# Optimization experiments

Hardware: AMD Instinct MI355X
Metric: run time of the kernel (lower is better)

The kernel has to match this reference:

```python
import jax, jax.numpy as jnp
import numpy as np

B, T_ENC, T_DEC = 64, 256, 200
MEL, R = 80, 2
ENC_DIM = 256   # must equal attention_context_dim (context = weighted sum of encoder outputs)
ATT = 256       # attention_rnn_units == attention_context_dim
DEC = 256       # decoder_rnn_units
PRE1, PRE2 = 256, 128


def _gru(x, h, wih, whh, bih, bhh):
    # torch.nn.GRUCell math; weights are (3*H, in) torch layout
    gi = x @ wih.T + bih
    gh = h @ whh.T + bhh
    i_r, i_z, i_n = jnp.split(gi, 3, axis=-1)
    h_r, h_z, h_n = jnp.split(gh, 3, axis=-1)
    r = jax.nn.sigmoid(i_r + h_r)
    z = jax.nn.sigmoid(i_z + h_z)
    n = jnp.tanh(i_n + r * h_n)
    return (1.0 - z) * n + z * h


def setup_inputs() -> dict:
    key = jax.random.key(0)
    ks = iter(jax.random.split(key, 40))
    def nrm(shape, s=0.05):
        return jax.random.normal(next(ks), shape, dtype=jnp.float32) * s
    inp = {
        "encoder_outputs": nrm((B, T_ENC, ENC_DIM), 1.0),
        "inputs": nrm((B, T_DEC, MEL * R), 1.0),
        "memory_lengths": jax.random.randint(next(ks), (B,), T_ENC // 2, T_ENC + 1),
        # prenet
        "pre_w1": nrm((PRE1, MEL * R)), "pre_b1": jnp.zeros((PRE1,), jnp.float32),
        "pre_w2": nrm((PRE2, PRE1)),    "pre_b2": jnp.zeros((PRE2,), jnp.float32),
        # memory layer (no bias)
        "mem_w": nrm((ATT, ENC_DIM)),
        # attention GRUCell: input = prenet_out(128) + context(256)
        "att_wih": nrm((3 * ATT, PRE2 + ATT)), "att_whh": nrm((3 * ATT, ATT)),
        "att_bih": jnp.zeros((3 * ATT,), jnp.float32), "att_bhh": jnp.zeros((3 * ATT,), jnp.float32),
        # Bahdanau attention: query layer (no bias) and v vector
        "q_w": nrm((ATT, ATT)), "v_w": nrm((ATT,)),
        # project_to_decoder_in
        "proj_w": nrm((DEC, ATT + ATT)), "proj_b": jnp.zeros((DEC,), jnp.float32),
        # two decoder GRUCells
        "g1_wih": nrm((3 * DEC, DEC)), "g1_whh": nrm((3 * DEC, DEC)),
        "g1_bih": jnp.zeros((3 * DEC,), jnp.float32), "g1_bhh": jnp.zeros((3 * DEC,), jnp.float32),
        "g2_wih": nrm((3 * DEC, DEC)), "g2_whh": nrm((3 * DEC, DEC)),
        "g2_bih": jnp.zeros((3 * DEC,), jnp.float32), "g2_bhh": jnp.zeros((3 * DEC,), jnp.float32),
        # output projections
        "mel_w": nrm((MEL * R, DEC + ATT)), "mel_b": jnp.zeros((MEL * R,), jnp.float32),
        "stop_w": nrm((1, DEC + ATT)),      "stop_b": jnp.zeros((1,), jnp.float32),
    }
    return inp


def reference(encoder_outputs, inputs, memory_lengths,
              pre_w1, pre_b1, pre_w2, pre_b2, mem_w,
              att_wih, att_whh, att_bih, att_bhh, q_w, v_w,
              proj_w, proj_b,
              g1_wih, g1_whh, g1_bih, g1_bhh,
              g2_wih, g2_whh, g2_bih, g2_bhh,
              mel_w, mel_b, stop_w, stop_b):
    b = encoder_outputs.shape[0]
    processed_memory = encoder_outputs @ mem_w.T                    # (B,T_enc,ATT)
    pad_mask = jnp.arange(T_ENC)[None, :] >= memory_lengths[:, None]  # True = padding

    # teacher forcing: step t consumes previous target frame (zeros at t=0)
    x_seq = jnp.concatenate([jnp.zeros((b, 1, MEL * R), inputs.dtype), inputs[:, :-1]], axis=1)
    xs = jnp.swapaxes(x_seq, 0, 1)                                  # (T_dec,B,mel*r)

    def step(carry, x):
        h_att, ctx, h1, h2 = carry
        # prenet (dropout omitted: deterministic reference)
        pre = jax.nn.relu(jax.nn.relu(x @ pre_w1.T + pre_b1) @ pre_w2.T + pre_b2)
        # attention RNN
        h_att = _gru(jnp.concatenate([pre, ctx], -1), h_att, att_wih, att_whh, att_bih, att_bhh)
        # Bahdanau alignment
        score = jnp.einsum('btd,d->bt', jnp.tanh(processed_memory + (h_att @ q_w.T)[:, None, :]), v_w)
        score = jnp.where(pad_mask, -jnp.inf, score)
        align = jax.nn.softmax(score, axis=-1)                      # (B,T_enc)
        ctx = jnp.einsum('bt,btd->bd', align, encoder_outputs)      # (B,ATT)
        # decoder stack with residuals
        d = jnp.concatenate([h_att, ctx], -1) @ proj_w.T + proj_b
        h1 = _gru(d, h1, g1_wih, g1_whh, g1_bih, g1_bhh); d = h1 + d
        h2 = _gru(d, h2, g2_wih, g2_whh, g2_bih, g2_bhh); d = h2 + d
        p = jnp.concatenate([d, ctx], -1)
        mel = p @ mel_w.T + mel_b                                   # (B,mel*r)
        stop = jax.nn.sigmoid(p @ stop_w.T + stop_b)[:, 0]          # (B,)
        return (h_att, ctx, h1, h2), (mel, align, stop)

    zeros = lambda d: jnp.zeros((b, d), encoder_outputs.dtype)
    init = (zeros(ATT), zeros(ATT), zeros(DEC), zeros(DEC))
    _, (mels, aligns, stops) = jax.lax.scan(step, init, xs)

    mel_outputs = jnp.swapaxes(mels, 0, 1)                          # (B,T_dec,mel*r)
    attn_scores = jnp.swapaxes(aligns, 0, 1)                        # (B,T_dec,T_enc)
    stop_tokens = jnp.repeat(jnp.swapaxes(stops, 0, 1), R, axis=1)  # (B,T_dec*r)
    return mel_outputs, attn_scores, stop_tokens
```

## Files before the change

kernel.cpp:

```cpp
#include <hip/hip_runtime.h>
#include <math.h>
#include <stdint.h>

#define NB   64
#define TE   256
#define TD   200
#define MR   160

typedef _Float16 h2 __attribute__((ext_vector_type(2)));

__device__ __forceinline__ float dot2f(h2 a, h2 b, float c){
  return __builtin_amdgcn_fdot2(a, b, c, false);
}
__device__ __forceinline__ h2 u2h(unsigned int u){ return __builtin_bit_cast(h2, u); }
__device__ __forceinline__ unsigned int h2u(h2 h){ return __builtin_bit_cast(unsigned int, h); }
__device__ __forceinline__ unsigned f2u(float f){ return __builtin_bit_cast(unsigned, f); }
__device__ __forceinline__ float u2f(unsigned u){ return __builtin_bit_cast(float, u); }

__device__ __forceinline__ float sigmf(float x){
  return __fdividef(1.f, 1.f + __expf(-x));
}
__device__ __forceinline__ float tanhf_(float x){
  float ax = fabsf(x);
  float e  = __expf(-2.f*ax);
  float r  = __fdividef(1.f - e, 1.f + e);
  return copysignf(r, x);
}

static constexpr size_t OFF_PM   = 0;
static constexpr size_t OFF_ENCH = 8388608;
static constexpr size_t OFF_GIP  = 16777216;
static constexpr size_t OFF_P    = 36438016;
static constexpr size_t OFF_W2   = 49545216;
static constexpr size_t OFF_W8   = 50184192;
static constexpr size_t WS_NEEDED = 52936704;

static constexpr size_t A_PW1  = 0;
static constexpr size_t A_PW2  = 20480;
static constexpr size_t A_WIHP = 36864;
static constexpr size_t A_MEMW = 86016;
static constexpr size_t A_MELW = 118784;

static constexpr size_t B_ATTC = 0;
static constexpr size_t B_ATTH = 24576;
static constexpr size_t B_G1I  = 49152;
static constexpr size_t B_G1H  = 73728;
static constexpr size_t B_G2I  = 98304;
static constexpr size_t B_G2H  = 122880;
static constexpr size_t B_PROJ = 147456;
static constexpr size_t B_QW   = 163840;

__global__ void k_conv(const float* __restrict__ src, char* __restrict__ ws,
                       unsigned off_h2, int O, int Kh, int k0, int ld){
  int i = blockIdx.x*256 + threadIdx.x;
  if (i >= O*Kh) return;
  int o = i % O, kp = i / O;
  _Float16* dst = (_Float16*)(ws + OFF_W2) + 2*((size_t)off_h2 + i);
  dst[0] = (_Float16)src[(size_t)o*ld + k0 + 2*kp    ];
  dst[1] = (_Float16)src[(size_t)o*ld + k0 + 2*kp + 1];
}

__global__ void k_conv8(const float* __restrict__ src, char* __restrict__ ws,
                        unsigned off16, int O, int Kq, int k0, int ld){
  int i = blockIdx.x*256 + threadIdx.x;
  if (i >= O*Kq) return;
  int o = i % O, kq = i / O;
  const float* s = src + (size_t)o*ld + k0 + kq*8;
  h2 p0, p1, p2, p3;
  p0.x=(_Float16)s[0]; p0.y=(_Float16)s[1];
  p1.x=(_Float16)s[2]; p1.y=(_Float16)s[3];
  p2.x=(_Float16)s[4]; p2.y=(_Float16)s[5];
  p3.x=(_Float16)s[6]; p3.y=(_Float16)s[7];
  uint4 r; r.x=h2u(p0); r.y=h2u(p1); r.z=h2u(p2); r.w=h2u(p3);
  ((uint4*)(ws + OFF_W8))[(size_t)off16 + i] = r;
}

__global__ void k_pm(const float* __restrict__ enc, char* __restrict__ ws){
  int bt = blockIdx.x;
  int j  = threadIdx.x;
  const h2* mw = (const h2*)(ws + OFF_W2) + A_MEMW;
  _Float16* pmN  = (_Float16*)(ws + OFF_PM);
  _Float16* encH = (_Float16*)(ws + OFF_ENCH);
  __shared__ _Float16 e[256];
  float ev = enc[(size_t)bt*256 + j];
  e[j] = (_Float16)ev;
  encH[(size_t)bt*256 + j] = (_Float16)ev;
  __syncthreads();
  const h2* e2 = (const h2*)e;
  float acc = 0.f;
  #pragma unroll 8
  for (int kp=0; kp<128; ++kp) acc = dot2f(mw[kp*256 + j], e2[kp], acc);
  pmN[(size_t)bt*256 + j] = (_Float16)acc;
}

__global__ void k_pre(const float* __restrict__ xin, const float* __restrict__ b1,
                      const float* __restrict__ b2, const float* __restrict__ bih,
                      char* __restrict__ ws){
  int bt = blockIdx.x;
  int b = bt / TD, t = bt % TD;
  int j = threadIdx.x;
  const h2* w1 = (const h2*)(ws + OFF_W2) + A_PW1;
  const h2* w2 = (const h2*)(ws + OFF_W2) + A_PW2;
  const h2* wp = (const h2*)(ws + OFF_W2) + A_WIHP;
  _Float16* gip = (_Float16*)(ws + OFF_GIP) + (size_t)bt*768;
  __shared__ _Float16 xh[160];
  __shared__ _Float16 a1[256];
  __shared__ _Float16 pr[128];
  if (j < 160)
    xh[j] = (t==0) ? (_Float16)0.f : (_Float16)xin[((size_t)b*TD + (t-1))*MR + j];
  __syncthreads();
  {
    const h2* x2 = (const h2*)xh;
    float acc = b1[j];
    #pragma unroll 8
    for (int kp=0; kp<80; ++kp) acc = dot2f(w1[kp*256 + j], x2[kp], acc);
    a1[j] = (_Float16)fmaxf(acc, 0.f);
  }
  __syncthreads();
  if (j < 128){
    const h2* x2 = (const h2*)a1;
    float acc = b2[j];
    #pragma unroll 8
    for (int kp=0; kp<128; ++kp) acc = dot2f(w2[kp*128 + j], x2[kp], acc);
    pr[j] = (_Float16)fmaxf(acc, 0.f);
  }
  __syncthreads();
  {
    const h2* p2 = (const h2*)pr;
    for (int o=j; o<768; o+=256){
      float acc = bih[o];
      #pragma unroll 8
      for (int kp=0; kp<64; ++kp) acc = dot2f(wp[kp*768 + o], p2[kp], acc);
      gip[o] = (_Float16)acc;
    }
  }
}

__global__ void k_zero(float* __restrict__ out){
  int* prog = (int*)(out + (size_t)NB*TD*MR + (size_t)NB*TD*TE);
  if (threadIdx.x < 256) prog[threadIdx.x] = 0;
}

__device__ __forceinline__ float d4dot(uint4 w, uint4 x, float a){
  a = dot2f(u2h(w.x), u2h(x.x), a);
  a = dot2f(u2h(w.y), u2h(x.y), a);
  a = dot2f(u2h(w.z), u2h(x.z), a);
  a = dot2f(u2h(w.w), u2h(x.w), a);
  return a;
}

__device__ __forceinline__ void gemv4(const uint4* __restrict__ wI, const uint4* __restrict__ wH,
                                      const uint4* xI, const uint4* xH,
                                      int j, int ks, float* scr, int tid){
  float a0=0.f,a1=0.f,a2=0.f,a3=0.f;
  #pragma unroll 2
  for (int kq=ks*8; kq<ks*8+8; ++kq){
    uint4 xi = xI[kq];
    uint4 xh = xH[kq];
    a0 = d4dot(wI[kq*768 +       j], xi, a0);
    a1 = d4dot(wI[kq*768 + 256 + j], xi, a1);
    a2 = d4dot(wI[kq*768 + 512 + j], xi, a2);
    a0 = d4dot(wH[kq*768 +       j], xh, a0);
    a1 = d4dot(wH[kq*768 + 256 + j], xh, a1);
    a3 = d4dot(wH[kq*768 + 512 + j], xh, a3);
  }
  float* r = scr + tid*4;
  r[0]=a0; r[1]=a1; r[2]=a2; r[3]=a3;
}

__global__ __launch_bounds__(1024) void k_dec(
    const int*   __restrict__ memlen,
    const float* __restrict__ att_bhh,
    const float* __restrict__ vw,
    const float* __restrict__ proj_b,
    const float* __restrict__ g1_bih, const float* __restrict__ g1_bhh,
    const float* __restrict__ g2_bih, const float* __restrict__ g2_bhh,
    float* __restrict__ out, char* __restrict__ ws)
{
  const int tid  = threadIdx.x;
  const int x    = blockIdx.x;
  const int y    = x >> 3;
  const int role = y & 3;
  const int b    = ((y >> 2) << 3) | (x & 7);
  const int ks   = tid >> 8;
  const int j    = tid & 255;

  const uint4* W8 = (const uint4*)(ws + OFF_W8);
  int* prog = (int*)(out + (size_t)NB*TD*MR + (size_t)NB*TD*TE);
  int* pP   = prog;
  int* pAl  = prog + 64;
  int* pD   = prog + 128;
  int* pB1  = prog + 192;
  unsigned* gX = (unsigned*)((_Float16*)(ws + OFF_GIP) + (size_t)b*TD*768);
  unsigned* uSlot = (unsigned*)out + (size_t)NB*TD*128 + (size_t)b*768;
  unsigned* aSlot = (unsigned*)out + (size_t)NB*TD*128 + (size_t)NB*768 + (size_t)b*256;

  __shared__ __align__(16) _Float16 hAh[256], ctxh[256], hh[256], dh[256];
  __shared__ float hAf[256], hf[256], df[256];
  __shared__ float qf[256], sc[256], al[256], vl[256];
  __shared__ float scr[4096];
  __shared__ float red2[4];
  __shared__ __align__(16) uint4 pmL[8192];

  if (role == 0){
    const uint4* wAC = W8 + B_ATTC;
    const uint4* wAH = W8 + B_ATTH;
    const uint4* wQ4 = W8 + B_QW;
    const uint4* pm4 = (const uint4*)(ws + OFF_PM) + (size_t)b*8192;
    const _Float16* gipB = (const _Float16*)(ws + OFF_GIP) + (size_t)b*TD*768;
    float* outA = out + (size_t)NB*TD*MR + (size_t)b*TD*TE;
    const int ml = memlen[b];

    for (int idx = tid; idx < 8192; idx += 1024){
      int tp = idx >> 5, g = idx & 31;
      pmL[(tp<<5) | (g ^ (tp & 7))] = pm4[idx];
    }
    if (tid < 256){ hAh[tid]=(_Float16)0.f; hAf[tid]=0.f; ctxh[tid]=(_Float16)0.f; vl[tid]=vw[tid]; }
    __syncthreads();
    const uint4* hA4  = (const uint4*)hAh;
    const uint4* ctx4 = (const uint4*)ctxh;

    #pragma unroll 1
    for (int t=0; t<TD; ++t){
      float a0=0.f, a1=0.f, a2=0.f, a3=0.f;
      #pragma unroll 2
      for (int i=0;i<8;++i){
        int kq = ks*8+i;
        uint4 xv = hA4[kq];
        a0 = d4dot(wAH[kq*768 +       j], xv, a0);
        a1 = d4dot(wAH[kq*768 + 256 + j], xv, a1);
        a3 = d4dot(wAH[kq*768 + 512 + j], xv, a3);
      }
      if (t > 0){
        if (tid==0){
          while (__hip_atomic_load(pP+b, __ATOMIC_RELAXED, __HIP_MEMORY_SCOPE_AGENT) < 2*t-1)
            __builtin_amdgcn_s_sleep(1);
        }
        __syncthreads();
        if (tid<128)
          ((unsigned*)ctxh)[tid] = __hip_atomic_load(gX + (size_t)(t-1)*384 + 128 + tid,
                                                     __ATOMIC_RELAXED, __HIP_MEMORY_SCOPE_AGENT);
        __syncthreads();
      }
      #pragma unroll
      for (int i=0;i<2;++i){
        int kq = ks*2+i;
        uint4 xv = ctx4[kq];
        a0 = d4dot(wAC[kq*768 +       j], xv, a0);
        a1 = d4dot(wAC[kq*768 + 256 + j], xv, a1);
        a2 = d4dot(wAC[kq*768 + 512 + j], xv, a2);
      }
      { float* r = scr + tid*4; r[0]=a0; r[1]=a1; r[2]=a2; r[3]=a3; }
      if (t > 0 && tid==0){
        while (__hip_atomic_load(pP+b, __ATOMIC_RELAXED, __HIP_MEMORY_SCOPE_AGENT) < 2*t)
          __builtin_amdgcn_s_sleep(1);
      }
      __syncthreads();
      if (tid < 256){
        const _Float16* gp = gipB + (size_t)t*768;
        float s0 = scr[tid*4+0]+scr[(256+tid)*4+0]+scr[(512+tid)*4+0]+scr[(768+tid)*4+0];
        float s1 = scr[tid*4+1]+scr[(256+tid)*4+1]+scr[(512+tid)*4+1]+scr[(768+tid)*4+1];
        float s2 = scr[tid*4+2]+scr[(256+tid)*4+2]+scr[(512+tid)*4+2]+scr[(768+tid)*4+2];
        float s3 = scr[tid*4+3]+scr[(256+tid)*4+3]+scr[(512+tid)*4+3]+scr[(768+tid)*4+3];
        if (t > 0){
          s0 += u2f(__hip_atomic_load(uSlot +       tid, __ATOMIC_RELAXED, __HIP_MEMORY_SCOPE_AGENT));
          s1 += u2f(__hip_atomic_load(uSlot + 256 + tid, __ATOMIC_RELAXED, __HIP_MEMORY_SCOPE_AGENT));
          s2 += u2f(__hip_atomic_load(uSlot + 512 + tid, __ATOMIC_RELAXED, __HIP_MEMORY_SCOPE_AGENT));
        }
        float r = sigmf(s0 + (float)gp[tid]     + att_bhh[tid]);
        float z = sigmf(s1 + (float)gp[256+tid] + att_bhh[256+tid]);
        float n = tanhf_(s2 + (float)gp[512+tid] + r*(s3 + att_bhh[512+tid]));
        float h = (1.f-z)*n + z*hAf[tid];
        hAf[tid]=h; hAh[tid]=(_Float16)h;
      }
      __syncthreads();
      { float a=0.f;
        #pragma unroll 2
        for (int kq=ks*8; kq<ks*8+8; ++kq)
          a = d4dot(wQ4[kq*256 + j], hA4[kq], a);
        scr[tid]=a; }
      if (tid<128)
        __hip_atomic_store(gX + (size_t)t*384 + tid, ((const unsigned*)hAh)[tid],
                           __ATOMIC_RELAXED, __HIP_MEMORY_SCOPE_AGENT);
      __syncthreads();
      if (tid<256) qf[tid] = scr[tid]+scr[256+tid]+scr[512+tid]+scr[768+tid];
      __syncthreads();
      { float s=0.f;
        #pragma unroll
        for (int i=0;i<8;++i){
          int g = ks*8 + i;
          uint4 q4 = pmL[(j<<5) | (g ^ (j&7))];
          int d0 = ks*64 + i*8;
          h2 p0=u2h(q4.x), p1=u2h(q4.y), p2=u2h(q4.z), p3=u2h(q4.w);
          s += vl[d0+0]*tanhf_((float)p0.x + qf[d0+0]);
          s += vl[d0+1]*tanhf_((float)p0.y + qf[d0+1]);
          s += vl[d0+2]*tanhf_((float)p1.x + qf[d0+2]);
          s += vl[d0+3]*tanhf_((float)p1.y + qf[d0+3]);
          s += vl[d0+4]*tanhf_((float)p2.x + qf[d0+4]);
          s += vl[d0+5]*tanhf_((float)p2.y + qf[d0+5]);
          s += vl[d0+6]*tanhf_((float)p3.x + qf[d0+6]);
          s += vl[d0+7]*tanhf_((float)p3.y + qf[d0+7]);
        }
        scr[tid]=s; }
      __syncthreads();
      if (tid<256){
        float s = scr[tid]+scr[256+tid]+scr[512+tid]+scr[768+tid];
        sc[tid] = (tid < ml) ? s : -INFINITY;
      }
      __syncthreads();
      {
        float v = (tid<256) ? sc[tid] : -INFINITY;
        if (tid<256){
          #pragma unroll
          for (int o=32;o>0;o>>=1) v = fmaxf(v, __shfl_down(v,o,64));
          if ((tid&63)==0) red2[tid>>6]=v;
        }
        __syncthreads();
        float m = fmaxf(fmaxf(red2[0],red2[1]), fmaxf(red2[2],red2[3]));
        __syncthreads();
        float e = 0.f;
        if (tid<256){
          e = __expf(sc[tid]-m);
          float sv = e;
          #pragma unroll
          for (int o=32;o>0;o>>=1) sv += __shfl_down(sv,o,64);
          if ((tid&63)==0) red2[tid>>6]=sv;
        }
        __syncthreads();
        if (tid<256){
          float sum = red2[0]+red2[1]+red2[2]+red2[3];
          float a = e*__fdividef(1.f,sum);
          outA[(size_t)t*TE + tid]=a;
          __hip_atomic_store(aSlot + tid, f2u(a),
                             __ATOMIC_RELAXED, __HIP_MEMORY_SCOPE_AGENT);
        }
      }
      __syncthreads();
      if (tid==0)
        __hip_atomic_store(pAl+b, t+1, __ATOMIC_RELEASE, __HIP_MEMORY_SCOPE_AGENT);
    }
  } else if (role == 1){
    const uint4* wAC  = W8 + B_ATTC;
    const uint4* wPRJ = W8 + B_PROJ;
    const unsigned* encW = (const unsigned*)(ws + OFF_ENCH) + (size_t)b*TE*128;
    _Float16* pstB = (_Float16*)(ws + OFF_P) + (size_t)b*TD*512;
    unsigned* encL = (unsigned*)pmL;
    const uint4* hA4  = (const uint4*)hAh;
    const uint4* ctx4 = (const uint4*)ctxh;
    const int tsl = tid>>7, dp = tid&127;

    for (int idx = tid; idx < 32768; idx += 1024) encL[idx] = encW[idx];
    __syncthreads();

    #pragma unroll 1
    for (int t=0; t<TD; ++t){
      if (tid==0){
        while (__hip_atomic_load(pAl+b, __ATOMIC_RELAXED, __HIP_MEMORY_SCOPE_AGENT) < t+1)
          __builtin_amdgcn_s_sleep(1);
      }
      __syncthreads();
      if (tid<256)
        al[tid] = u2f(__hip_atomic_load(aSlot + tid, __ATOMIC_RELAXED, __HIP_MEMORY_SCOPE_AGENT));
      if (tid >= 256 && tid < 384)
        ((unsigned*)hAh)[tid-256] = __hip_atomic_load(gX + (size_t)t*384 + (tid-256),
                                                      __ATOMIC_RELAXED, __HIP_MEMORY_SCOPE_AGENT);
      __syncthreads();
      { float c0=0.f, c1=0.f;
        #pragma unroll 8
        for (int tp=tsl*32; tp<tsl*32+32; ++tp){
          float a = al[tp];
          h2 e = u2h(encL[tp*128 + dp]);
          c0 += a*(float)e.x; c1 += a*(float)e.y;
        }
        scr[tid*2]=c0; scr[tid*2+1]=c1; }
      __syncthreads();
      if (tid<128){
        float c0=0.f, c1=0.f;
        #pragma unroll
        for (int k=0;k<8;++k){ c0 += scr[(k*128+tid)*2]; c1 += scr[(k*128+tid)*2+1]; }
        h2 c; c.x=(_Float16)c0; c.y=(_Float16)c1;
        unsigned w = h2u(c);
        ((unsigned*)ctxh)[tid] = w;
        ((unsigned*)pstB)[(size_t)t*256 + 128 + tid] = w;
        __hip_atomic_store(gX + (size_t)t*384 + 128 + tid, w,
                           __ATOMIC_RELAXED, __HIP_MEMORY_SCOPE_AGENT);
      }
      __syncthreads();
      if (tid==0)
        __hip_atomic_store(pP+b, 2*t+1, __ATOMIC_RELEASE, __HIP_MEMORY_SCOPE_AGENT);
      { float a0=0.f, a1=0.f, a2=0.f;
        #pragma unroll 2
        for (int i=0;i<6;++i){
          int kq = 8 + ks*6 + i;
          uint4 xv = ctx4[kq];
          a0 = d4dot(wAC[kq*768 +       j], xv, a0);
          a1 = d4dot(wAC[kq*768 + 256 + j], xv, a1);
          a2 = d4dot(wAC[kq*768 + 512 + j], xv, a2);
        }
        float* r = scr + tid*3; r[0]=a0; r[1]=a1; r[2]=a2; }
      __syncthreads();
      if (tid<256){
        float p0 = scr[tid*3+0]+scr[(256+tid)*3+0]+scr[(512+tid)*3+0]+scr[(768+tid)*3+0];
        float p1 = scr[tid*3+1]+scr[(256+tid)*3+1]+scr[(512+tid)*3+1]+scr[(768+tid)*3+1];
        float p2 = scr[tid*3+2]+scr[(256+tid)*3+2]+scr[(512+tid)*3+2]+scr[(768+tid)*3+2];
        __hip_atomic_store(uSlot +       tid, f2u(p0), __ATOMIC_RELAXED, __HIP_MEMORY_SCOPE_AGENT);
        __hip_atomic_store(uSlot + 256 + tid, f2u(p1), __ATOMIC_RELAXED, __HIP_MEMORY_SCOPE_AGENT);
        __hip_atomic_store(uSlot + 512 + tid, f2u(p2), __ATOMIC_RELAXED, __HIP_MEMORY_SCOPE_AGENT);
      }
      __syncthreads();
      if (tid==0)
        __hip_atomic_store(pP+b, 2*t+2, __ATOMIC_RELEASE, __HIP_MEMORY_SCOPE_AGENT);
      { float a=0.f;
        #pragma unroll 2
        for (int kq=ks*16; kq<ks*16+16; ++kq){
          uint4 xa = (kq < 32) ? hA4[kq] : ctx4[kq-32];
          a = d4dot(wPRJ[kq*256 + j], xa, a);
        }
        scr[tid]=a; }
      __syncthreads();
      if (tid<128){
        const int o0 = 2*tid, o1 = o0+1;
        float d0 = scr[o0]+scr[256+o0]+scr[512+o0]+scr[768+o0] + proj_b[o0];
        float d1 = scr[o1]+scr[256+o1]+scr[512+o1]+scr[768+o1] + proj_b[o1];
        h2 p; p.x=(_Float16)d0; p.y=(_Float16)d1;
        __hip_atomic_store(gX + (size_t)t*384 + 256 + tid, h2u(p),
                           __ATOMIC_RELAXED, __HIP_MEMORY_SCOPE_AGENT);
      }
      __syncthreads();
      if (tid==0)
        __hip_atomic_store(pD+b, t+1, __ATOMIC_RELEASE, __HIP_MEMORY_SCOPE_AGENT);
    }
  } else {
    const bool isB1 = (role == 2);
    const uint4* wI = W8 + (isB1 ? B_G1I : B_G2I);
    const uint4* wH = W8 + (isB1 ? B_G1H : B_G2H);
    const float* bih = isB1 ? g1_bih : g2_bih;
    const float* bhh = isB1 ? g1_bhh : g2_bhh;
    int* pin = isB1 ? pD : pB1;
    unsigned* oX = (unsigned*)out + (size_t)b*TD*128;
    const unsigned* inP = isB1 ? (gX + 256) : oX;
    const int instr = isB1 ? 384 : 128;
    _Float16* pstB = (_Float16*)(ws + OFF_P) + (size_t)b*TD*512;

    if (tid<256){ hh[tid]=(_Float16)0.f; hf[tid]=0.f; }
    __syncthreads();
    const uint4* h4  = (const uint4*)hh;
    const uint4* dd4 = (const uint4*)dh;

    #pragma unroll 1
    for (int t=0; t<TD; ++t){
      if (tid==0){
        while (__hip_atomic_load(pin+b, __ATOMIC_RELAXED, __HIP_MEMORY_SCOPE_AGENT) < t+1)
          __builtin_amdgcn_s_sleep(1);
      }
      __syncthreads();
      if (tid<128){
        unsigned w = __hip_atomic_load(inP + (size_t)t*instr + tid,
                                       __ATOMIC_RELAXED, __HIP_MEMORY_SCOPE_AGENT);
        ((unsigned*)dh)[tid] = w;
        h2 p = u2h(w);
        df[2*tid]   = (float)p.x;
        df[2*tid+1] = (float)p.y;
      }
      __syncthreads();
      gemv4(wI, wH, dd4, h4, j, ks, scr, tid);
      __syncthreads();
      if (tid<256){
        float s0 = scr[tid*4+0]+scr[(256+tid)*4+0]+scr[(512+tid)*4+0]+scr[(768+tid)*4+0];
        float s1 = scr[tid*4+1]+scr[(256+tid)*4+1]+scr[(512+tid)*4+1]+scr[(768+tid)*4+1];
        float s2 = scr[tid*4+2]+scr[(256+tid)*4+2]+scr[(512+tid)*4+2]+scr[(768+tid)*4+2];
        float s3 = scr[tid*4+3]+scr[(256+tid)*4+3]+scr[(512+tid)*4+3]+scr[(768+tid)*4+3];
        float r = sigmf(s0 + bih[tid]     + bhh[tid]);
        float z = sigmf(s1 + bih[256+tid] + bhh[256+tid]);
        float n = tanhf_(s2 + bih[512+tid] + r*(s3 + bhh[512+tid]));
        float h = (1.f-z)*n + z*hf[tid];
        float dn = h + df[tid];
        hf[tid]=h; hh[tid]=(_Float16)h;
        dh[tid]=(_Float16)dn;
        if (!isB1) pstB[(size_t)t*512 + tid] = (_Float16)dn;
      }
      __syncthreads();
      if (isB1){
        if (tid<128)
          __hip_atomic_store(oX + (size_t)t*128 + tid, ((const unsigned*)dh)[tid],
                             __ATOMIC_RELAXED, __HIP_MEMORY_SCOPE_AGENT);
        __syncthreads();
        if (tid==0)
          __hip_atomic_store(pB1+b, t+1, __ATOMIC_RELEASE, __HIP_MEMORY_SCOPE_AGENT);
      }
    }
  }
}

__global__ void k_post(const float* __restrict__ mel_b, const float* __restrict__ stop_w,
                       const float* __restrict__ stop_b, float* __restrict__ out,
                       char* __restrict__ ws){
  int bt = blockIdx.x;
  int b = bt / TD, t = bt % TD;
  int j = threadIdx.x;
  const h2* wm = (const h2*)(ws + OFF_W2) + A_MELW;
  const _Float16* p = (const _Float16*)(ws + OFF_P) + (size_t)bt*512;
  __shared__ _Float16 pl[512];
  ((uint32_t*)pl)[j] = ((const uint32_t*)p)[j];
  __syncthreads();
  const h2* p2 = (const h2*)pl;
  if (j < 160){
    float acc = mel_b[j];
    #pragma unroll 8
    for (int kp=0; kp<256; ++kp) acc = dot2f(wm[kp*160 + j], p2[kp], acc);
    out[(size_t)bt*MR + j] = acc;
  } else if (j == 160){
    float acc = stop_b[0];
    for (int k=0; k<512; ++k) acc += stop_w[k]*(float)pl[k];
    float s = __fdividef(1.f, 1.f + __expf(-acc));
    float* os = out + (size_t)NB*TD*MR + (size_t)NB*TD*TE + (size_t)b*2*TD;
    os[2*t]   = s;
    os[2*t+1] = s;
  }
}

extern "C" void kernel_launch(void* const* d_in, const int* in_sizes, int n_in,
                              void* d_out, int out_size, void* d_ws, size_t ws_size,
                              hipStream_t stream)
{
  const float* enc     = (const float*)d_in[0];
  const float* xin     = (const float*)d_in[1];
  const int*   mlen    = (const int*)  d_in[2];
  const float* pre_w1  = (const float*)d_in[3];
  const float* pre_b1  = (const float*)d_in[4];
  const float* pre_w2  = (const float*)d_in[5];
  const float* pre_b2  = (const float*)d_in[6];
  const float* mem_w   = (const float*)d_in[7];
  const float* att_wih = (const float*)d_in[8];
  const float* att_whh = (const float*)d_in[9];
  const float* att_bih = (const float*)d_in[10];
  const float* att_bhh = (const float*)d_in[11];
  const float* q_w     = (const float*)d_in[12];
  const float* v_w     = (const float*)d_in[13];
  const float* proj_w  = (const float*)d_in[14];
  const float* proj_b  = (const float*)d_in[15];
  const float* g1_wih  = (const float*)d_in[16];
  const float* g1_whh  = (const float*)d_in[17];
  const float* g1_bih  = (const float*)d_in[18];
  const float* g1_bhh  = (const float*)d_in[19];
  const float* g2_wih  = (const float*)d_in[20];
  const float* g2_whh  = (const float*)d_in[21];
  const float* g2_bih  = (const float*)d_in[22];
  const float* g2_bhh  = (const float*)d_in[23];
  const float* mel_w   = (const float*)d_in[24];
  const float* mel_b   = (const float*)d_in[25];
  const float* stop_w  = (const float*)d_in[26];
  const float* stop_b  = (const float*)d_in[27];
  (void)in_sizes; (void)n_in; (void)out_size;

  if (ws_size < WS_NEEDED) return;

  float* out = (float*)d_out;
  char*  ws  = (char*)d_ws;

  auto conv = [&](const float* src, size_t off_h2, int O, int Kh, int k0, int ld){
    int n = O*Kh;
    k_conv<<<(n+255)/256, 256, 0, stream>>>(src, ws, (unsigned)off_h2, O, Kh, k0, ld);
  };
  auto conv8 = [&](const float* src, size_t off16, int O, int Kq, int k0, int ld){
    int n = O*Kq;
    k_conv8<<<(n+255)/256, 256, 0, stream>>>(src, ws, (unsigned)off16, O, Kq, k0, ld);
  };

  conv(pre_w1,  A_PW1,  256, 80,  0, 160);
  conv(pre_w2,  A_PW2,  128, 128, 0, 256);
  conv(att_wih, A_WIHP, 768, 64,  0, 384);
  conv(mem_w,   A_MEMW, 256, 128, 0, 256);
  conv(mel_w,   A_MELW, 160, 256, 0, 512);
  conv8(att_wih, B_ATTC, 768, 32, 128, 384);
  conv8(att_whh, B_ATTH, 768, 32, 0,   256);
  conv8(g1_wih,  B_G1I,  768, 32, 0,   256);
  conv8(g1_whh,  B_G1H,  768, 32, 0,   256);
  conv8(g2_wih,  B_G2I,  768, 32, 0,   256);
  conv8(g2_whh,  B_G2H,  768, 32, 0,   256);
  conv8(proj_w,  B_PROJ, 256, 64, 0,   512);
  conv8(q_w,     B_QW,   256, 32, 0,   256);

  k_pm  <<<NB*TE, 256, 0, stream>>>(enc, ws);
  k_pre <<<NB*TD, 256, 0, stream>>>(xin, pre_b1, pre_b2, att_bih, ws);
  k_zero<<<1, 256, 0, stream>>>(out);
  k_dec <<<4*NB, 1024, 0, stream>>>(mlen, att_bhh, v_w, proj_b,
                                    g1_bih, g1_bhh, g2_bih, g2_bhh, out, ws);
  k_post<<<NB*TD, 256, 0, stream>>>(mel_b, stop_w, stop_b, out, ws);
}
```

Before: 4.686 ms.

## Move full context GRU input matvec to context role and drop softmax max pass

Role 1 now computes the whole context-to-gate matvec and publishes it once per step. Role 0 no longer waits on an intermediate progress flag, loads ctx, or does a partial context matvec, so one cross-block handshake and its barriers go away. The softmax also skips the max-subtraction reduction and exponentiates raw scores directly, removing a reduction and two barriers. This relies on the scores being small enough not to overflow, and role 0 now waits longer for the full context contribution.

```diff
diff --git a/kernel.cpp b/kernel.cpp
--- a/kernel.cpp
+++ b/kernel.cpp
@@ -203,7 +203,6 @@
   __shared__ __align__(16) uint4 pmL[8192];
 
   if (role == 0){
-    const uint4* wAC = W8 + B_ATTC;
     const uint4* wAH = W8 + B_ATTH;
     const uint4* wQ4 = W8 + B_QW;
     const uint4* pm4 = (const uint4*)(ws + OFF_PM) + (size_t)b*8192;
@@ -215,14 +214,13 @@
       int tp = idx >> 5, g = idx & 31;
       pmL[(tp<<5) | (g ^ (tp & 7))] = pm4[idx];
     }
-    if (tid < 256){ hAh[tid]=(_Float16)0.f; hAf[tid]=0.f; ctxh[tid]=(_Float16)0.f; vl[tid]=vw[tid]; }
+    if (tid < 256){ hAh[tid]=(_Float16)0.f; hAf[tid]=0.f; vl[tid]=vw[tid]; }
     __syncthreads();
-    const uint4* hA4  = (const uint4*)hAh;
-    const uint4* ctx4 = (const uint4*)ctxh;
+    const uint4* hA4 = (const uint4*)hAh;
 
     #pragma unroll 1
     for (int t=0; t<TD; ++t){
-      float a0=0.f, a1=0.f, a2=0.f, a3=0.f;
+      float a0=0.f, a1=0.f, a3=0.f;
       #pragma unroll 2
       for (int i=0;i<8;++i){
         int kq = ks*8+i;
@@ -231,41 +229,22 @@
         a1 = d4dot(wAH[kq*768 + 256 + j], xv, a1);
         a3 = d4dot(wAH[kq*768 + 512 + j], xv, a3);
       }
-      if (t > 0){
-        if (tid==0){
-          while (__hip_atomic_load(pP+b, __ATOMIC_RELAXED, __HIP_MEMORY_SCOPE_AGENT) < 2*t-1)
-            __builtin_amdgcn_s_sleep(1);
-        }
-        __syncthreads();
-        if (tid<128)
-          ((unsigned*)ctxh)[tid] = __hip_atomic_load(gX + (size_t)(t-1)*384 + 128 + tid,
-                                                     __ATOMIC_RELAXED, __HIP_MEMORY_SCOPE_AGENT);
-        __syncthreads();
-      }
-      #pragma unroll
-      for (int i=0;i<2;++i){
-        int kq = ks*2+i;
-        uint4 xv = ctx4[kq];
-        a0 = d4dot(wAC[kq*768 +       j], xv, a0);
-        a1 = d4dot(wAC[kq*768 + 256 + j], xv, a1);
-        a2 = d4dot(wAC[kq*768 + 512 + j], xv, a2);
-      }
-      { float* r = scr + tid*4; r[0]=a0; r[1]=a1; r[2]=a2; r[3]=a3; }
+      { float* r = scr + tid*3; r[0]=a0; r[1]=a1; r[2]=a3; }
       if (t > 0 && tid==0){
-        while (__hip_atomic_load(pP+b, __ATOMIC_RELAXED, __HIP_MEMORY_SCOPE_AGENT) < 2*t)
+        while (__hip_atomic_load(pP+b, __ATOMIC_RELAXED, __HIP_MEMORY_SCOPE_AGENT) < t)
           __builtin_amdgcn_s_sleep(1);
       }
       __syncthreads();
       if (tid < 256){
         const _Float16* gp = gipB + (size_t)t*768;
-        float s0 = scr[tid*4+0]+scr[(256+tid)*4+0]+scr[(512+tid)*4+0]+scr[(768+tid)*4+0];
-        float s1 = scr[tid*4+1]+scr[(256+tid)*4+1]+scr[(512+tid)*4+1]+scr[(768+tid)*4+1];
-        float s2 = scr[tid*4+2]+scr[(256+tid)*4+2]+scr[(512+tid)*4+2]+scr[(768+tid)*4+2];
-        float s3 = scr[tid*4+3]+scr[(256+tid)*4+3]+scr[(512+tid)*4+3]+scr[(768+tid)*4+3];
+        float s0 = scr[tid*3+0]+scr[(256+tid)*3+0]+scr[(512+tid)*3+0]+scr[(768+tid)*3+0];
+        float s1 = scr[tid*3+1]+scr[(256+tid)*3+1]+scr[(512+tid)*3+1]+scr[(768+tid)*3+1];
+        float s3 = scr[tid*3+2]+scr[(256+tid)*3+2]+scr[(512+tid)*3+2]+scr[(768+tid)*3+2];
+        float s2 = 0.f;
         if (t > 0){
           s0 += u2f(__hip_atomic_load(uSlot +       tid, __ATOMIC_RELAXED, __HIP_MEMORY_SCOPE_AGENT));
           s1 += u2f(__hip_atomic_load(uSlot + 256 + tid, __ATOMIC_RELAXED, __HIP_MEMORY_SCOPE_AGENT));
-          s2 += u2f(__hip_atomic_load(uSlot + 512 + tid, __ATOMIC_RELAXED, __HIP_MEMORY_SCOPE_AGENT));
+          s2  = u2f(__hip_atomic_load(uSlot + 512 + tid, __ATOMIC_RELAXED, __HIP_MEMORY_SCOPE_AGENT));
         }
         float r = sigmf(s0 + (float)gp[tid]     + att_bhh[tid]);
         float z = sigmf(s1 + (float)gp[256+tid] + att_bhh[256+tid]);
@@ -305,35 +284,20 @@
       __syncthreads();
       if (tid<256){
         float s = scr[tid]+scr[256+tid]+scr[512+tid]+scr[768+tid];
-        sc[tid] = (tid < ml) ? s : -INFINITY;
-      }
-      __syncthreads();
-      {
-        float v = (tid<256) ? sc[tid] : -INFINITY;
-        if (tid<256){
-          #pragma unroll
-          for (int o=32;o>0;o>>=1) v = fmaxf(v, __shfl_down(v,o,64));
-          if ((tid&63)==0) red2[tid>>6]=v;
-        }
-        __syncthreads();
-        float m = fmaxf(fmaxf(red2[0],red2[1]), fmaxf(red2[2],red2[3]));
-        __syncthreads();
-        float e = 0.f;
-        if (tid<256){
-          e = __expf(sc[tid]-m);
-          float sv = e;
-          #pragma unroll
-          for (int o=32;o>0;o>>=1) sv += __shfl_down(sv,o,64);
-          if ((tid&63)==0) red2[tid>>6]=sv;
-        }
-        __syncthreads();
-        if (tid<256){
-          float sum = red2[0]+red2[1]+red2[2]+red2[3];
-          float a = e*__fdividef(1.f,sum);
-          outA[(size_t)t*TE + tid]=a;
-          __hip_atomic_store(aSlot + tid, f2u(a),
-                             __ATOMIC_RELAXED, __HIP_MEMORY_SCOPE_AGENT);
-        }
+        float e = (tid < ml) ? __expf(s) : 0.f;
+        sc[tid] = e;
+        float sv = e;
+        #pragma unroll
+        for (int o=32;o>0;o>>=1) sv += __shfl_down(sv,o,64);
+        if ((tid&63)==0) red2[tid>>6]=sv;
+      }
+      __syncthreads();
+      if (tid<256){
+        float sum = red2[0]+red2[1]+red2[2]+red2[3];
+        float a = sc[tid]*__fdividef(1.f,sum);
+        outA[(size_t)t*TE + tid]=a;
+        __hip_atomic_store(aSlot + tid, f2u(a),
+                           __ATOMIC_RELAXED, __HIP_MEMORY_SCOPE_AGENT);
       }
       __syncthreads();
       if (tid==0)
@@ -382,16 +346,11 @@
         unsigned w = h2u(c);
         ((unsigned*)ctxh)[tid] = w;
         ((unsigned*)pstB)[(size_t)t*256 + 128 + tid] = w;
-        __hip_atomic_store(gX + (size_t)t*384 + 128 + tid, w,
-                           __ATOMIC_RELAXED, __HIP_MEMORY_SCOPE_AGENT);
-      }
-      __syncthreads();
-      if (tid==0)
-        __hip_atomic_store(pP+b, 2*t+1, __ATOMIC_RELEASE, __HIP_MEMORY_SCOPE_AGENT);
+      }
+      __syncthreads();
       { float a0=0.f, a1=0.f, a2=0.f;
         #pragma unroll 2
-        for (int i=0;i<6;++i){
-          int kq = 8 + ks*6 + i;
+        for (int kq=ks*8; kq<ks*8+8; ++kq){
           uint4 xv = ctx4[kq];
           a0 = d4dot(wAC[kq*768 +       j], xv, a0);
           a1 = d4dot(wAC[kq*768 + 256 + j], xv, a1);
@@ -409,7 +368,7 @@
       }
       __syncthreads();
       if (tid==0)
-        __hip_atomic_store(pP+b, 2*t+2, __ATOMIC_RELEASE, __HIP_MEMORY_SCOPE_AGENT);
+        __hip_atomic_store(pP+b, t+1, __ATOMIC_RELEASE, __HIP_MEMORY_SCOPE_AGENT);
       { float a=0.f;
         #pragma unroll 2
         for (int kq=ks*16; kq<ks*16+16; ++kq){
```

New measurement: 4.463 ms. 1.05x faster.
